# Optimization experiments

Measured on AMD Instinct MI355X. Metric: run time of the kernel, lower is better.

The kernel has to match this reference:

```python
import jax, jax.numpy as jnp
import numpy as np

EPS = 1e-6

def _rms_norm(x, w):
    # torch: x / (||x||_2 * n^{-1/2} + eps) * w
    rms = jnp.linalg.norm(x, axis=-1, keepdims=True) * (x.shape[-1] ** -0.5)
    return x / (rms + EPS) * w

def _rope_cos_sin(seq_len, head_dim):
    half = head_dim // 2
    freq = 1.0 / (10000.0 ** (jnp.arange(half, dtype=jnp.float32) / half))
    t = jnp.arange(seq_len, dtype=jnp.float32)
    freqs = t[:, None] * freq[None, :]            # [s, half]
    freqs = jnp.concatenate([freqs, freqs], -1)   # [s, d_head]
    cos = jnp.cos(freqs)[None, :, None, :]        # [1, s, 1, d_head]
    sin = jnp.sin(freqs)[None, :, None, :]
    return cos, sin

def _rotate_half(x):
    h = x.shape[-1] // 2
    return jnp.concatenate([-x[..., h:], x[..., :h]], -1)

def setup_inputs() -> dict:
    key = jax.random.key(0)
    ks = jax.random.split(key, 8)
    B, S, D, H, F = 2, 2048, 2048, 16, 128
    return {
        'query_input': jax.random.normal(ks[0], (B, S, D), jnp.float32),
        'key_input':   jax.random.normal(ks[1], (B, S, D), jnp.float32),
        'value_input': jax.random.normal(ks[2], (B, S, D), jnp.float32),
        'W_Q': jax.random.normal(ks[3], (H, D, F), jnp.float32) * (D ** -0.5),
        'W_K': jax.random.normal(ks[4], (H, D, F), jnp.float32) * (D ** -0.5),
        'W_V': jax.random.normal(ks[5], (H, D, F), jnp.float32) * (D ** -0.5),
        'W_O': jax.random.normal(ks[6], (H, F, D), jnp.float32) * (F ** -0.5),
        'b_Q': jnp.zeros((H, F), jnp.float32),
        'b_K': jnp.zeros((H, F), jnp.float32),
        'b_V': jnp.zeros((H, F), jnp.float32),
        'b_O': jnp.zeros((D,), jnp.float32),
        'q_norm_w': jnp.ones((F,), jnp.float32),
        'k_norm_w': jnp.ones((F,), jnp.float32),
    }

def reference(query_input, key_input, value_input, W_Q, W_K, W_V, W_O,
              b_Q, b_K, b_V, b_O, q_norm_w, k_norm_w):
    head_dim = W_Q.shape[-1]
    q = jnp.einsum('bpd,hdf->bphf', query_input, W_Q) + b_Q[None, None]
    k = jnp.einsum('bpd,hdf->bphf', key_input,   W_K) + b_K[None, None]
    v = jnp.einsum('bpd,hdf->bphf', value_input, W_V) + b_V[None, None]
    q = _rms_norm(q, q_norm_w)
    k = _rms_norm(k, k_norm_w)
    cos, sin = _rope_cos_sin(q.shape[1], head_dim)
    q = q * cos + _rotate_half(q) * sin
    k = k * cos + _rotate_half(k) * sin
    scores = jnp.einsum('bphf,bqhf->bhpq', q, k) / (head_dim ** 0.5)
    pattern = jax.nn.softmax(scores, axis=-1)
    attn = jnp.einsum('bhpq,bqhf->bphf', pattern, v)
    return jnp.einsum('bphf,hfm->bpm', attn, W_O) + b_O
```

## Files before the change

kernel.cpp:

```cpp
#include <hip/hip_runtime.h>
#include <stdint.h>

typedef unsigned short u16;
typedef __attribute__((ext_vector_type(8))) short  s8b;
typedef __attribute__((ext_vector_type(4))) float  f32x4;

#define S_LEN   2048
#define NHEAD   16
#define HD      128
#define DM      2048
#define NB      2
#define NPLANE  (NB*NHEAD)
#define ROWS    (NB*S_LEN)
#define PLANE_ELEMS (S_LEN*HD)
#define ATT_SCALE 0.08838834764831845f
#define LOG2E     1.4426950408889634f

__device__ __forceinline__ float bf2f(u16 u){
  union { unsigned u; float f; } x; x.u = ((unsigned)u) << 16; return x.f;
}
__device__ __forceinline__ u16 f2bf(float f){
  union { float f; unsigned u; } x; x.f = f;
  unsigned r = x.u + 0x7FFFu + ((x.u >> 16) & 1u);
  return (u16)(r >> 16);
}
__device__ __forceinline__ unsigned cvtpk(float lo, float hi){
  unsigned r;
  asm("v_cvt_pk_bf16_f32 %0, %1, %2" : "=v"(r) : "v"(lo), "v"(hi));
  return r;
}

typedef const __attribute__((address_space(1))) unsigned int* gas1;
typedef __attribute__((address_space(3))) unsigned int* las3;
__device__ __forceinline__ void gload16(const void* g, void* l){
  __builtin_amdgcn_global_load_lds((gas1)g, (las3)l, 16, 0, 0);
}

__device__ __forceinline__ f32x4 mfma16(s8b a, s8b b, f32x4 c){
  return __builtin_amdgcn_mfma_f32_16x16x32_bf16(a, b, c, 0, 0, 0);
}

__global__ __launch_bounds__(256) void cvt4x3(const float4* __restrict__ a,
                                              const float4* __restrict__ b,
                                              const float4* __restrict__ c,
                                              uint2* __restrict__ oa,
                                              uint2* __restrict__ ob,
                                              uint2* __restrict__ oc, int n4){
  int i = blockIdx.x*256 + threadIdx.x;
  if (i >= n4) return;
  const float4* src = (blockIdx.y == 0) ? a : (blockIdx.y == 1) ? b : c;
  uint2*       dst  = (blockIdx.y == 0) ? oa : (blockIdx.y == 1) ? ob : oc;
  float4 v = src[i];
  uint2 o;
  o.x = (unsigned)f2bf(v.x) | ((unsigned)f2bf(v.y) << 16);
  o.y = (unsigned)f2bf(v.z) | ((unsigned)f2bf(v.w) << 16);
  dst[i] = o;
}

__global__ __launch_bounds__(256) void transpose_cvt(const float* __restrict__ in,
                                                     u16* __restrict__ out,
                                                     int R, int C, int outStride){
  __shared__ float tile[32][33];
  int z = blockIdx.z;
  const float* inz = in + (size_t)z * R * C;
  u16* outz = out + (size_t)z * C * outStride;
  int r0 = blockIdx.x*32, c0 = blockIdx.y*32;
  int tx = threadIdx.x, ty = threadIdx.y;
  #pragma unroll
  for (int i=0;i<4;i++)
    tile[ty*4+i][tx] = inz[(size_t)(r0+ty*4+i)*C + c0 + tx];
  __syncthreads();
  #pragma unroll
  for (int i=0;i<4;i++)
    outz[(size_t)(c0+ty*4+i)*outStride + r0 + tx] = f2bf(tile[tx][ty*4+i]);
}

__global__ __launch_bounds__(256) void rope_tab(float* __restrict__ ctab,
                                                float* __restrict__ stab){
  int i = blockIdx.x*256 + threadIdx.x;
  int p = i >> 6, j = i & 63;
  float freq = exp2f(-(float)j * (13.287712379549449f/64.0f));
  float a = (float)p * freq;
  ctab[i] = cosf(a);
  stab[i] = sinf(a);
}

__global__ __launch_bounds__(512) void gemm_bt(const u16* __restrict__ A,
                                               const u16* __restrict__ BT,
                                               const float* __restrict__ bias,
                                               void* __restrict__ out, int mode){
  const int K = 2048;
  const int NT = 32;
  __shared__ u16 lds[6*12288];
  const int t = threadIdx.x, w = t >> 6, l = t & 63;
  const int lr = l & 15, lg = l >> 4;
  const int wr = w >> 1, wc = w & 1;
  int bid = blockIdx.x;
  int swz = (bid & 7)*32 + (bid >> 3);
  const int M0 = (swz >> 4) * 256, N0 = (swz & 15) * 128;

  f32x4 acc[4][4];
  #pragma unroll
  for (int i=0;i<4;i++)
    #pragma unroll
    for (int j=0;j<4;j++) acc[i][j] = f32x4{0.f,0.f,0.f,0.f};

  auto stageH = [&](int ttu, int h){
    int slot = (2*ttu + h) % 6;
    int tt   = ttu & 31;
    char* base = (char*)&lds[slot*12288];
    #pragma unroll
    for (int j=0;j<2;j++){
      int d = w*2048 + j*1024 + l*16;
      int row = d >> 7;
      int koff = ((l&7)*16) ^ ((row&7)<<4);
      gload16((const char*)A + ((size_t)(M0 + h*128 + row)*K + tt*64)*2 + koff,
              base + w*2048 + j*1024);
    }
    {
      int d = w*1024 + l*16;
      int row = d >> 7;
      int koff = ((l&7)*16) ^ ((row&7)<<4);
      gload16((const char*)BT + ((size_t)(N0 + h*64 + row)*K + tt*64)*2 + koff,
              base + 16384 + w*1024);
    }
  };

  stageH(0,0); stageH(0,1); stageH(1,0); stageH(1,1);

  for (int kt=0; kt<NT; kt++){
    const char* Ab = (const char*)&lds[((2*kt + (wr>>1)) % 6)*12288];
    const char* Bb = (const char*)&lds[((2*kt + wc) % 6)*12288] + 16384;

    stageH(kt+2, 0);
    asm volatile("s_waitcnt vmcnt(9)" ::: "memory");
    __builtin_amdgcn_s_barrier();
    __builtin_amdgcn_sched_barrier(0);

    s8b af[4][2];
    #pragma unroll
    for (int mi=0;mi<4;mi++)
      #pragma unroll
      for (int kc=0;kc<2;kc++){
        int rA = (wr&1)*64 + mi*16 + lr;
        af[mi][kc] = *(const s8b*)(Ab + rA*128 + ((kc*64 + lg*16) ^ ((rA&7)<<4)));
      }
    {
      s8b bf0, bf1;
      int rB = 0*16 + lr;
      bf0 = *(const s8b*)(Bb + rB*128 + ((0*64 + lg*16) ^ ((rB&7)<<4)));
      bf1 = *(const s8b*)(Bb + rB*128 + ((1*64 + lg*16) ^ ((rB&7)<<4)));
      __builtin_amdgcn_s_setprio(1);
      #pragma unroll
      for (int mi=0;mi<4;mi++){
        acc[mi][0] = mfma16(af[mi][0], bf0, acc[mi][0]);
        acc[mi][0] = mfma16(af[mi][1], bf1, acc[mi][0]);
      }
      __builtin_amdgcn_s_setprio(0);
    }
    {
      s8b bf0, bf1;
      int rB = 1*16 + lr;
      bf0 = *(const s8b*)(Bb + rB*128 + ((0*64 + lg*16) ^ ((rB&7)<<4)));
      bf1 = *(const s8b*)(Bb + rB*128 + ((1*64 + lg*16) ^ ((rB&7)<<4)));
      __builtin_amdgcn_s_setprio(1);
      #pragma unroll
      for (int mi=0;mi<4;mi++){
        acc[mi][1] = mfma16(af[mi][0], bf0, acc[mi][1]);
        acc[mi][1] = mfma16(af[mi][1], bf1, acc[mi][1]);
      }
      __builtin_amdgcn_s_setprio(0);
    }
    __builtin_amdgcn_sched_barrier(0);
    __builtin_amdgcn_s_barrier();
    __builtin_amdgcn_sched_barrier(0);
    stageH(kt+2, 1);
    {
      s8b bf0, bf1;
      int rB = 2*16 + lr;
      bf0 = *(const s8b*)(Bb + rB*128 + ((0*64 + lg*16) ^ ((rB&7)<<4)));
      bf1 = *(const s8b*)(Bb + rB*128 + ((1*64 + lg*16) ^ ((rB&7)<<4)));
      __builtin_amdgcn_s_setprio(1);
      #pragma unroll
      for (int mi=0;mi<4;mi++){
        acc[mi][2] = mfma16(af[mi][0], bf0, acc[mi][2]);
        acc[mi][2] = mfma16(af[mi][1], bf1, acc[mi][2]);
      }
      __builtin_amdgcn_s_setprio(0);
    }
    {
      s8b bf0, bf1;
      int rB = 3*16 + lr;
      bf0 = *(const s8b*)(Bb + rB*128 + ((0*64 + lg*16) ^ ((rB&7)<<4)));
      bf1 = *(const s8b*)(Bb + rB*128 + ((1*64 + lg*16) ^ ((rB&7)<<4)));
      __builtin_amdgcn_s_setprio(1);
      #pragma unroll
      for (int mi=0;mi<4;mi++){
        acc[mi][3] = mfma16(af[mi][0], bf0, acc[mi][3]);
        acc[mi][3] = mfma16(af[mi][1], bf1, acc[mi][3]);
      }
      __builtin_amdgcn_s_setprio(0);
    }
    __builtin_amdgcn_sched_barrier(0);
    __builtin_amdgcn_s_barrier();
    __builtin_amdgcn_sched_barrier(0);
  }
  asm volatile("s_waitcnt vmcnt(0)" ::: "memory");

  #pragma unroll
  for (int mi=0;mi<4;mi++){
    int growb = M0 + wr*64 + mi*16 + lg*4;
    #pragma unroll
    for (int nj=0;nj<4;nj++){
      int gcol = N0 + wc*64 + nj*16 + lr;
      float bv = bias[gcol];
      #pragma unroll
      for (int r=0;r<4;r++){
        int grow = growb + r;
        float v = acc[mi][nj][r] + bv;
        if (mode == 2){
          ((float*)out)[(size_t)grow*2048 + gcol] = v;
        } else {
          int b = grow >> 11, p = grow & 2047;
          int h = gcol >> 7,  f = gcol & 127;
          if (mode == 0){
            ((u16*)out)[(((size_t)(b*NHEAD+h))*S_LEN + p)*HD + f] = f2bf(v);
          } else {
            size_t base = ((size_t)(b*NHEAD+h)*PLANE_ELEMS + (size_t)(p>>6)*8192) * 2;
            int p6 = p & 63;
            int q_ = ((p6&12)<<1) | (p6&3) | ((p6&16)>>2);
            int kvp = (p6 & 32) | q_;
            int byte = (f*128 + kvp*2) ^ ((f&7)<<4);
            *(u16*)((char*)out + base + byte) = f2bf(v);
          }
        }
      }
    }
  }
}

__global__ __launch_bounds__(256) void norm_rope(const u16* __restrict__ in,
                                                 u16* __restrict__ outp,
                                                 const float* __restrict__ nw,
                                                 const float* __restrict__ ctab,
                                                 const float* __restrict__ stab,
                                                 int swizzled, float oscale){
  int t = threadIdx.x, w = t>>6, l = t&63;
  size_t R = (size_t)blockIdx.x*4 + w;
  int p = (int)(R & (S_LEN-1));
  size_t base = R * HD;
  float x0 = bf2f(in[base + l]);
  float x1 = bf2f(in[base + 64 + l]);
  float ss = x0*x0 + x1*x1;
  #pragma unroll
  for (int m=1;m<64;m<<=1) ss += __shfl_xor(ss, m);
  float rms = sqrtf(ss * (1.0f/128.0f));
  float sc = oscale / (rms + 1e-6f);
  float xn0 = x0 * sc * nw[l];
  float xn1 = x1 * sc * nw[64+l];
  float c = ctab[(size_t)p*64 + l], s = stab[(size_t)p*64 + l];
  float o0 = xn0*c - xn1*s;
  float o1 = xn1*c + xn0*s;
  if (!swizzled){
    outp[base + l]      = f2bf(o0);
    outp[base + 64 + l] = f2bf(o1);
  } else {
    size_t plane = R >> 11;
    int kv = p & 63;
    size_t tb = (plane*(size_t)PLANE_ELEMS + (size_t)(p>>6)*8192) * 2;
    int b0 = (kv*256 + l*2)        ^ ((kv&7)<<4);
    int b1 = (kv*256 + (64+l)*2)   ^ ((kv&7)<<4);
    *(u16*)((char*)outp + tb + b0) = f2bf(o0);
    *(u16*)((char*)outp + tb + b1) = f2bf(o1);
  }
}

__global__ __launch_bounds__(256,2) void attn_fwd(const u16* __restrict__ qn,
                                                  const u16* __restrict__ kn,
                                                  const u16* __restrict__ vt,
                                                  u16* __restrict__ attn_out){
  __shared__ u16 Klds[2][8192];
  __shared__ u16 Vlds[2][8192];
  int t = threadIdx.x, w = t>>6, l = t&63;
  int lr = l&15, lg = l>>4;

  int bid = blockIdx.x;
  int xcd = bid & 7, j = bid >> 3;
  int plane = xcd*4 + (j >> 4);
  int qb = j & 15;
  int q0 = qb*128 + w*32;

  s8b qf[2][4];
  #pragma unroll
  for (int qi=0; qi<2; qi++)
    #pragma unroll
    for (int fc=0; fc<4; fc++)
      qf[qi][fc] = *(const s8b*)(qn + ((size_t)plane*S_LEN + q0 + qi*16 + lr)*HD + fc*32 + lg*8);

  float m[2], lsum[2];
  #pragma unroll
  for (int qi=0;qi<2;qi++){ m[qi] = -1e30f; lsum[qi] = 0.f; }
  f32x4 oacc[2][8];
  #pragma unroll
  for (int qi=0;qi<2;qi++)
    #pragma unroll
    for (int i=0;i<8;i++) oacc[qi][i] = f32x4{0.f,0.f,0.f,0.f};

  const u16* kbase = kn + (size_t)plane*PLANE_ELEMS;
  const u16* vbase = vt + (size_t)plane*PLANE_ELEMS;

  auto stage = [&](int buf, int kt){
    #pragma unroll
    for (int i=0;i<4;i++){
      gload16(kbase + (size_t)kt*8192 + w*2048 + i*512 + l*8, &Klds[buf][w*2048 + i*512]);
      gload16(vbase + (size_t)kt*8192 + w*2048 + i*512 + l*8, &Vlds[buf][w*2048 + i*512]);
    }
  };

  stage(0, 0);
  int cur = 0;
  for (int kt=0; kt<32; kt++){
    __syncthreads();
    if (kt+1 < 32) stage(cur^1, kt+1);

    f32x4 sacc[4][2];
    #pragma unroll
    for (int c=0;c<4;c++)
      #pragma unroll
      for (int qi=0;qi<2;qi++) sacc[c][qi] = f32x4{0.f,0.f,0.f,0.f};
    __builtin_amdgcn_s_setprio(1);
    #pragma unroll
    for (int c=0;c<4;c++){
      int kv = c*16 + lr;
      #pragma unroll
      for (int fc=0; fc<4; fc++){
        int byte = (kv*256 + (fc*32 + lg*8)*2) ^ ((kv&7)<<4);
        s8b kf = *(const s8b*)((const char*)&Klds[cur][0] + byte);
        sacc[c][0] = mfma16(kf, qf[0][fc], sacc[c][0]);
        sacc[c][1] = mfma16(kf, qf[1][fc], sacc[c][1]);
      }
    }
    __builtin_amdgcn_s_setprio(0);

    float mx[2];
    #pragma unroll
    for (int qi=0;qi<2;qi++){
      float a0 = fmaxf(fmaxf(sacc[0][qi][0], sacc[0][qi][1]), fmaxf(sacc[0][qi][2], sacc[0][qi][3]));
      float a1 = fmaxf(fmaxf(sacc[1][qi][0], sacc[1][qi][1]), fmaxf(sacc[1][qi][2], sacc[1][qi][3]));
      float a2 = fmaxf(fmaxf(sacc[2][qi][0], sacc[2][qi][1]), fmaxf(sacc[2][qi][2], sacc[2][qi][3]));
      float a3 = fmaxf(fmaxf(sacc[3][qi][0], sacc[3][qi][1]), fmaxf(sacc[3][qi][2], sacc[3][qi][3]));
      mx[qi] = fmaxf(fmaxf(a0, a1), fmaxf(a2, a3));
    }
    bool need = (mx[0] > m[0] + 11.5f) || (mx[1] > m[1] + 11.5f);
    if (__any(need)){
      #pragma unroll
      for (int qi=0;qi<2;qi++){
        float v = mx[qi];
        v = fmaxf(v, __shfl_xor(v, 16));
        v = fmaxf(v, __shfl_xor(v, 32));
        v = fmaxf(m[qi], v);
        float al = exp2f(m[qi] - v);
        m[qi] = v; lsum[qi] *= al;
        float alr[4];
        #pragma unroll
        for (int r=0;r<4;r++) alr[r] = __shfl(al, lg*4 + r);
        #pragma unroll
        for (int i=0;i<8;i++)
          #pragma unroll
          for (int r=0;r<4;r++) oacc[qi][i][r] *= alr[r];
      }
    }
    float pv[2][4][4];
    #pragma unroll
    for (int qi=0;qi<2;qi++){
      float ls0=0.f, ls1=0.f, ls2=0.f, ls3=0.f;
      #pragma unroll
      for (int c=0;c<4;c++){
        float e0 = exp2f(sacc[c][qi][0] - m[qi]);
        float e1 = exp2f(sacc[c][qi][1] - m[qi]);
        float e2 = exp2f(sacc[c][qi][2] - m[qi]);
        float e3 = exp2f(sacc[c][qi][3] - m[qi]);
        pv[qi][c][0]=e0; pv[qi][c][1]=e1; pv[qi][c][2]=e2; pv[qi][c][3]=e3;
        ls0 += e0; ls1 += e1; ls2 += e2; ls3 += e3;
      }
      lsum[qi] += (ls0 + ls1) + (ls2 + ls3);
    }

    s8b pa[2][2];
    #pragma unroll
    for (int qi=0;qi<2;qi++)
      #pragma unroll
      for (int kc=0;kc<2;kc++){
        union { s8b v; unsigned u[4]; } pu;
        pu.u[0] = cvtpk(pv[qi][2*kc][0],   pv[qi][2*kc][1]);
        pu.u[1] = cvtpk(pv[qi][2*kc][2],   pv[qi][2*kc][3]);
        pu.u[2] = cvtpk(pv[qi][2*kc+1][0], pv[qi][2*kc+1][1]);
        pu.u[3] = cvtpk(pv[qi][2*kc+1][2], pv[qi][2*kc+1][3]);
        pa[qi][kc] = pu.v;
      }

    __builtin_amdgcn_s_setprio(1);
    #pragma unroll
    for (int kc=0;kc<2;kc++){
      #pragma unroll
      for (int fc2=0; fc2<8; fc2++){
        int f = fc2*16 + lr;
        int byte = (f*128 + (kc*32 + lg*8)*2) ^ ((f&7)<<4);
        s8b vf = *(const s8b*)((const char*)&Vlds[cur][0] + byte);
        oacc[0][fc2] = mfma16(pa[0][kc], vf, oacc[0][fc2]);
        oacc[1][fc2] = mfma16(pa[1][kc], vf, oacc[1][fc2]);
      }
    }
    __builtin_amdgcn_s_setprio(0);
    cur ^= 1;
  }

  int b = plane >> 4, h = plane & 15;
  #pragma unroll
  for (int qi=0;qi<2;qi++){
    float v = lsum[qi];
    v += __shfl_xor(v, 16);
    v += __shfl_xor(v, 32);
    v = 1.0f / v;
    float lir[4];
    #pragma unroll
    for (int r=0;r<4;r++) lir[r] = __shfl(v, lg*4 + r);
    #pragma unroll
    for (int fc2=0; fc2<8; fc2++){
      int f = fc2*16 + lr;
      #pragma unroll
      for (int r=0;r<4;r++){
        int row = q0 + qi*16 + lg*4 + r;
        float o = oacc[qi][fc2][r] * lir[r];
        attn_out[(((size_t)b*S_LEN + row)*NHEAD + h)*HD + f] = f2bf(o);
      }
    }
  }
}

extern "C" void kernel_launch(void* const* d_in, const int* in_sizes, int n_in,
                              void* d_out, int out_size, void* d_ws, size_t ws_size,
                              hipStream_t stream){
  const float* xq = (const float*)d_in[0];
  const float* xk = (const float*)d_in[1];
  const float* xv = (const float*)d_in[2];
  const float* WQ = (const float*)d_in[3];
  const float* WK = (const float*)d_in[4];
  const float* WV = (const float*)d_in[5];
  const float* WO = (const float*)d_in[6];
  const float* bQ = (const float*)d_in[7];
  const float* bK = (const float*)d_in[8];
  const float* bV = (const float*)d_in[9];
  const float* bO = (const float*)d_in[10];
  const float* qw = (const float*)d_in[11];
  const float* kw = (const float*)d_in[12];

  char* ws = (char*)d_ws;
  size_t off = 0;
  auto alloc = [&](size_t bytes)->void*{
    void* p = ws + off; off += (bytes + 255) & ~(size_t)255; return p;
  };
  const size_t ACT = (size_t)ROWS*DM*2;
  const size_t WMT = (size_t)DM*DM*2;
  u16* xqb  = (u16*)alloc(ACT);
  u16* xkb  = (u16*)alloc(ACT);
  u16* xvb  = (u16*)alloc(ACT);
  u16* WqT  = (u16*)alloc(WMT);
  u16* WkT  = (u16*)alloc(WMT);
  u16* WvT  = (u16*)alloc(WMT);
  u16* WoT  = (u16*)alloc(WMT);
  u16* qraw = (u16*)alloc(ACT);
  u16* kraw = (u16*)alloc(ACT);
  u16* knT  = (u16*)alloc(ACT);
  u16* vtS  = (u16*)alloc(ACT);
  u16* attn = (u16*)alloc(ACT);
  float* ctab = (float*)alloc((size_t)S_LEN*64*4);
  float* stab = (float*)alloc((size_t)S_LEN*64*4);
  if (off > ws_size) return;

  const int n4 = ROWS*DM/4;
  cvt4x3<<<dim3(n4/256, 3), dim3(256), 0, stream>>>((const float4*)xq, (const float4*)xk,
                                                    (const float4*)xv, (uint2*)xqb,
                                                    (uint2*)xkb, (uint2*)xvb, n4);
  rope_tab<<<dim3(S_LEN*64/256), dim3(256), 0, stream>>>(ctab, stab);
  transpose_cvt<<<dim3(64,4,16), dim3(32,8), 0, stream>>>(WQ, WqT, 2048, 128, 2048);
  transpose_cvt<<<dim3(64,4,16), dim3(32,8), 0, stream>>>(WK, WkT, 2048, 128, 2048);
  transpose_cvt<<<dim3(64,4,16), dim3(32,8), 0, stream>>>(WV, WvT, 2048, 128, 2048);
  transpose_cvt<<<dim3(64,64,1), dim3(32,8), 0, stream>>>(WO, WoT, 2048, 2048, 2048);

  gemm_bt<<<dim3(256), dim3(512), 0, stream>>>(xqb, WqT, bQ, qraw, 0);
  gemm_bt<<<dim3(256), dim3(512), 0, stream>>>(xkb, WkT, bK, kraw, 0);
  gemm_bt<<<dim3(256), dim3(512), 0, stream>>>(xvb, WvT, bV, vtS, 1);

  norm_rope<<<dim3(NPLANE*S_LEN/4), dim3(256), 0, stream>>>(qraw, qraw, qw, ctab, stab, 0, ATT_SCALE*LOG2E);
  norm_rope<<<dim3(NPLANE*S_LEN/4), dim3(256), 0, stream>>>(kraw, knT, kw, ctab, stab, 1, 1.0f);

  attn_fwd<<<dim3(512), dim3(256), 0, stream>>>(qraw, knT, vtS, attn);

  gemm_bt<<<dim3(256), dim3(512), 0, stream>>>(attn, WoT, bO, d_out, 2);
}
```

Baseline: 352.1 us.

## Fold max subtraction into MFMA init, compute row sums via MFMA, merge GEMM barriers

The attention kernel now starts the score accumulators at -m, so the running max is already subtracted and the per-element subtraction before exp2 disappears. The softmax denominator is accumulated with an extra MFMA against a ones vector instead of scalar adds and cross-lane shuffles. The projection GEMM loop merges its four B-column blocks into two and drops one of its three workgroup barriers per k-step. This trades VALU work for a few extra MFMAs, and the bf16-rounded P values now feed the denominator; removing the barrier between the two halves could risk a race with stageH overwriting LDS.

```diff
diff --git a/kernel.cpp b/kernel.cpp
--- a/kernel.cpp
+++ b/kernel.cpp
@@ -146,59 +146,40 @@
         af[mi][kc] = *(const s8b*)(Ab + rA*128 + ((kc*64 + lg*16) ^ ((rA&7)<<4)));
       }
     {
-      s8b bf0, bf1;
-      int rB = 0*16 + lr;
-      bf0 = *(const s8b*)(Bb + rB*128 + ((0*64 + lg*16) ^ ((rB&7)<<4)));
-      bf1 = *(const s8b*)(Bb + rB*128 + ((1*64 + lg*16) ^ ((rB&7)<<4)));
+      s8b bf[2][2];
+      #pragma unroll
+      for (int nj=0;nj<2;nj++){
+        int rB = nj*16 + lr;
+        bf[nj][0] = *(const s8b*)(Bb + rB*128 + ((0*64 + lg*16) ^ ((rB&7)<<4)));
+        bf[nj][1] = *(const s8b*)(Bb + rB*128 + ((1*64 + lg*16) ^ ((rB&7)<<4)));
+      }
       __builtin_amdgcn_s_setprio(1);
       #pragma unroll
-      for (int mi=0;mi<4;mi++){
-        acc[mi][0] = mfma16(af[mi][0], bf0, acc[mi][0]);
-        acc[mi][0] = mfma16(af[mi][1], bf1, acc[mi][0]);
-      }
+      for (int mi=0;mi<4;mi++)
+        #pragma unroll
+        for (int nj=0;nj<2;nj++){
+          acc[mi][nj] = mfma16(af[mi][0], bf[nj][0], acc[mi][nj]);
+          acc[mi][nj] = mfma16(af[mi][1], bf[nj][1], acc[mi][nj]);
+        }
       __builtin_amdgcn_s_setprio(0);
     }
-    {
-      s8b bf0, bf1;
-      int rB = 1*16 + lr;
-      bf0 = *(const s8b*)(Bb + rB*128 + ((0*64 + lg*16) ^ ((rB&7)<<4)));
-      bf1 = *(const s8b*)(Bb + rB*128 + ((1*64 + lg*16) ^ ((rB&7)<<4)));
-      __builtin_amdgcn_s_setprio(1);
-      #pragma unroll
-      for (int mi=0;mi<4;mi++){
-        acc[mi][1] = mfma16(af[mi][0], bf0, acc[mi][1]);
-        acc[mi][1] = mfma16(af[mi][1], bf1, acc[mi][1]);
-      }
-      __builtin_amdgcn_s_setprio(0);
-    }
-    __builtin_amdgcn_sched_barrier(0);
-    __builtin_amdgcn_s_barrier();
-    __builtin_amdgcn_sched_barrier(0);
     stageH(kt+2, 1);
     {
-      s8b bf0, bf1;
-      int rB = 2*16 + lr;
-      bf0 = *(const s8b*)(Bb + rB*128 + ((0*64 + lg*16) ^ ((rB&7)<<4)));
-      bf1 = *(const s8b*)(Bb + rB*128 + ((1*64 + lg*16) ^ ((rB&7)<<4)));
+      s8b bf[2][2];
+      #pragma unroll
+      for (int nj=0;nj<2;nj++){
+        int rB = (nj+2)*16 + lr;
+        bf[nj][0] = *(const s8b*)(Bb + rB*128 + ((0*64 + lg*16) ^ ((rB&7)<<4)));
+        bf[nj][1] = *(const s8b*)(Bb + rB*128 + ((1*64 + lg*16) ^ ((rB&7)<<4)));
+      }
       __builtin_amdgcn_s_setprio(1);
       #pragma unroll
-      for (int mi=0;mi<4;mi++){
-        acc[mi][2] = mfma16(af[mi][0], bf0, acc[mi][2]);
-        acc[mi][2] = mfma16(af[mi][1], bf1, acc[mi][2]);
-      }
-      __builtin_amdgcn_s_setprio(0);
-    }
-    {
-      s8b bf0, bf1;
-      int rB = 3*16 + lr;
-      bf0 = *(const s8b*)(Bb + rB*128 + ((0*64 + lg*16) ^ ((rB&7)<<4)));
-      bf1 = *(const s8b*)(Bb + rB*128 + ((1*64 + lg*16) ^ ((rB&7)<<4)));
-      __builtin_amdgcn_s_setprio(1);
-      #pragma unroll
-      for (int mi=0;mi<4;mi++){
-        acc[mi][3] = mfma16(af[mi][0], bf0, acc[mi][3]);
-        acc[mi][3] = mfma16(af[mi][1], bf1, acc[mi][3]);
-      }
+      for (int mi=0;mi<4;mi++)
+        #pragma unroll
+        for (int nj=0;nj<2;nj++){
+          acc[mi][nj+2] = mfma16(af[mi][0], bf[nj][0], acc[mi][nj+2]);
+          acc[mi][nj+2] = mfma16(af[mi][1], bf[nj][1], acc[mi][nj+2]);
+        }
       __builtin_amdgcn_s_setprio(0);
     }
     __builtin_amdgcn_sched_barrier(0);
@@ -290,6 +271,9 @@
   int qb = j & 15;
   int q0 = qb*128 + w*32;
 
+  const s8b ones = { (short)0x3F80, (short)0x3F80, (short)0x3F80, (short)0x3F80,
+                     (short)0x3F80, (short)0x3F80, (short)0x3F80, (short)0x3F80 };
+
   s8b qf[2][4];
   #pragma unroll
   for (int qi=0; qi<2; qi++)
@@ -297,9 +281,11 @@
     for (int fc=0; fc<4; fc++)
       qf[qi][fc] = *(const s8b*)(qn + ((size_t)plane*S_LEN + q0 + qi*16 + lr)*HD + fc*32 + lg*8);
 
-  float m[2], lsum[2];
-  #pragma unroll
-  for (int qi=0;qi<2;qi++){ m[qi] = -1e30f; lsum[qi] = 0.f; }
+  float m[2];
+  m[0] = 0.f; m[1] = 0.f;
+  f32x4 lacc[2];
+  lacc[0] = f32x4{0.f,0.f,0.f,0.f};
+  lacc[1] = f32x4{0.f,0.f,0.f,0.f};
   f32x4 oacc[2][8];
   #pragma unroll
   for (int qi=0;qi<2;qi++)
@@ -325,9 +311,10 @@
 
     f32x4 sacc[4][2];
     #pragma unroll
-    for (int c=0;c<4;c++)
-      #pragma unroll
-      for (int qi=0;qi<2;qi++) sacc[c][qi] = f32x4{0.f,0.f,0.f,0.f};
+    for (int c=0;c<4;c++){
+      sacc[c][0] = f32x4{-m[0],-m[0],-m[0],-m[0]};
+      sacc[c][1] = f32x4{-m[1],-m[1],-m[1],-m[1]};
+    }
     __builtin_amdgcn_s_setprio(1);
     #pragma unroll
     for (int c=0;c<4;c++){
@@ -351,16 +338,20 @@
       float a3 = fmaxf(fmaxf(sacc[3][qi][0], sacc[3][qi][1]), fmaxf(sacc[3][qi][2], sacc[3][qi][3]));
       mx[qi] = fmaxf(fmaxf(a0, a1), fmaxf(a2, a3));
     }
-    bool need = (mx[0] > m[0] + 11.5f) || (mx[1] > m[1] + 11.5f);
+    bool need = (mx[0] > 11.5f) || (mx[1] > 11.5f);
     if (__any(need)){
       #pragma unroll
       for (int qi=0;qi<2;qi++){
         float v = mx[qi];
         v = fmaxf(v, __shfl_xor(v, 16));
         v = fmaxf(v, __shfl_xor(v, 32));
-        v = fmaxf(m[qi], v);
-        float al = exp2f(m[qi] - v);
-        m[qi] = v; lsum[qi] *= al;
+        float delta = fmaxf(v, 0.f);
+        float al = exp2f(-delta);
+        m[qi] += delta;
+        #pragma unroll
+        for (int c=0;c<4;c++)
+          #pragma unroll
+          for (int r=0;r<4;r++) sacc[c][qi][r] -= delta;
         float alr[4];
         #pragma unroll
         for (int r=0;r<4;r++) alr[r] = __shfl(al, lg*4 + r);
@@ -368,23 +359,20 @@
         for (int i=0;i<8;i++)
           #pragma unroll
           for (int r=0;r<4;r++) oacc[qi][i][r] *= alr[r];
+        #pragma unroll
+        for (int r=0;r<4;r++) lacc[qi][r] *= alr[r];
       }
     }
     float pv[2][4][4];
     #pragma unroll
-    for (int qi=0;qi<2;qi++){
-      float ls0=0.f, ls1=0.f, ls2=0.f, ls3=0.f;
+    for (int qi=0;qi<2;qi++)
       #pragma unroll
       for (int c=0;c<4;c++){
-        float e0 = exp2f(sacc[c][qi][0] - m[qi]);
-        float e1 = exp2f(sacc[c][qi][1] - m[qi]);
-        float e2 = exp2f(sacc[c][qi][2] - m[qi]);
-        float e3 = exp2f(sacc[c][qi][3] - m[qi]);
-        pv[qi][c][0]=e0; pv[qi][c][1]=e1; pv[qi][c][2]=e2; pv[qi][c][3]=e3;
-        ls0 += e0; ls1 += e1; ls2 += e2; ls3 += e3;
-      }
-      lsum[qi] += (ls0 + ls1) + (ls2 + ls3);
-    }
+        pv[qi][c][0] = exp2f(sacc[c][qi][0]);
+        pv[qi][c][1] = exp2f(sacc[c][qi][1]);
+        pv[qi][c][2] = exp2f(sacc[c][qi][2]);
+        pv[qi][c][3] = exp2f(sacc[c][qi][3]);
+      }
 
     s8b pa[2][2];
     #pragma unroll
@@ -402,6 +390,8 @@
     __builtin_amdgcn_s_setprio(1);
     #pragma unroll
     for (int kc=0;kc<2;kc++){
+      lacc[0] = mfma16(pa[0][kc], ones, lacc[0]);
+      lacc[1] = mfma16(pa[1][kc], ones, lacc[1]);
       #pragma unroll
       for (int fc2=0; fc2<8; fc2++){
         int f = fc2*16 + lr;
@@ -418,20 +408,16 @@
   int b = plane >> 4, h = plane & 15;
   #pragma unroll
   for (int qi=0;qi<2;qi++){
-    float v = lsum[qi];
-    v += __shfl_xor(v, 16);
-    v += __shfl_xor(v, 32);
-    v = 1.0f / v;
-    float lir[4];
-    #pragma unroll
-    for (int r=0;r<4;r++) lir[r] = __shfl(v, lg*4 + r);
+    float inv[4];
+    #pragma unroll
+    for (int r=0;r<4;r++) inv[r] = 1.0f / lacc[qi][r];
     #pragma unroll
     for (int fc2=0; fc2<8; fc2++){
       int f = fc2*16 + lr;
       #pragma unroll
       for (int r=0;r<4;r++){
         int row = q0 + qi*16 + lg*4 + r;
-        float o = oacc[qi][fc2][r] * lir[r];
+        float o = oacc[qi][fc2][r] * inv[r];
         attn_out[(((size_t)b*S_LEN + row)*NHEAD + h)*HD + f] = f2bf(o);
       }
     }
```

Measured after the change: 346.4 us. No clear change (-1.6%).
